# Performance work log

Hardware: AMD Instinct MI355X
Metric: run time of the kernel (lower is better)

The kernel has to match this reference:

```python
import jax, jax.numpy as jnp
import numpy as np


def _gat_layer(x, W, att_l, att_r, b, src, dst, num_nodes, heads, out_feat, concat):
    # x: [N, in], W: [in, H*F]
    xl = (x @ W).reshape(num_nodes, heads, out_feat)          # [N, H, F]
    a_l = jnp.sum(xl * att_l, axis=2)                          # [N, H]
    a_r = jnp.sum(xl * att_r, axis=2)                          # [N, H]
    # edge scores: alpha_j (source, att_l) + alpha_i (target, att_r)
    e = a_l[src] + a_r[dst]                                    # [E, H]
    e = jax.nn.leaky_relu(e, 0.2)
    # segment softmax over destination-node neighborhoods
    e_max = jax.ops.segment_max(e, dst, num_segments=num_nodes)
    e_exp = jnp.exp(e - e_max[dst])
    denom = jax.ops.segment_sum(e_exp, dst, num_segments=num_nodes)
    alpha = e_exp / (denom[dst] + 1e-16)                       # [E, H]
    # weighted gather + scatter-add aggregation
    msg = alpha[:, :, None] * xl[src]                          # [E, H, F]
    out = jax.ops.segment_sum(msg, dst, num_segments=num_nodes)  # [N, H, F]
    if concat:
        out = out.reshape(num_nodes, heads * out_feat)
    else:
        out = out.mean(axis=1)                                 # [N, F]
    return out + b


def setup_inputs() -> dict:
    key = jax.random.key(0)
    ks = jax.random.split(key, 8)
    N, E = 50000, 800000
    in_dim, hidden, out_dim, H = 128, 8, 64, 8
    x = jax.random.normal(ks[0], (N, in_dim), dtype=jnp.float32)
    edge_index = jax.random.randint(ks[1], (2, E), 0, N, dtype=jnp.int64)
    s = 0.1
    return {
        "x": x,
        "edge_index": edge_index,
        "W1": jax.random.normal(ks[2], (in_dim, hidden * H), dtype=jnp.float32) * s,
        "att_l1": jax.random.normal(ks[3], (1, H, hidden), dtype=jnp.float32) * s,
        "att_r1": jax.random.normal(ks[4], (1, H, hidden), dtype=jnp.float32) * s,
        "b1": jnp.zeros((hidden * H,), dtype=jnp.float32),
        "W2": jax.random.normal(ks[5], (hidden * H, out_dim * H), dtype=jnp.float32) * s,
        "att_l2": jax.random.normal(ks[6], (1, H, out_dim), dtype=jnp.float32) * s,
        "att_r2": jax.random.normal(ks[7], (1, H, out_dim), dtype=jnp.float32) * s,
        "b2": jnp.zeros((1, out_dim), dtype=jnp.float32),
    }


def reference(x, edge_index, W1, att_l1, att_r1, b1, W2, att_l2, att_r2, b2):
    N = x.shape[0]
    H = att_l1.shape[1]
    src, dst = edge_index[0], edge_index[1]
    h = _gat_layer(x, W1, att_l1, att_r1, b1, src, dst, N, H, att_l1.shape[2], concat=True)
    h = jax.nn.relu(h)
    out = _gat_layer(h, W2, att_l2, att_r2, b2, src, dst, N, H, att_l2.shape[2], concat=False)
    return out
```

## Files before the change

### kernel.cpp

```cpp
#include <hip/hip_runtime.h>
#include <stdint.h>

#define NT 256

typedef __attribute__((ext_vector_type(8))) short bf16x8;
typedef __attribute__((ext_vector_type(4))) float f32x4;

__device__ __forceinline__ float lrelu(float x) { return x > 0.f ? x : 0.2f * x; }

__device__ __forceinline__ float b2f(unsigned short u) {
  union { unsigned int i; float f; } v; v.i = ((unsigned int)u) << 16; return v.f;
}
__device__ __forceinline__ unsigned short f2b(float f) {
  unsigned int u = __float_as_uint(f);
  return (unsigned short)((u + 0x7fffu + ((u >> 16) & 1u)) >> 16);
}

__global__ void detect_kernel(const int* __restrict__ ei, int* __restrict__ flag, int twoE) {
  __shared__ int any;
  if (threadIdx.x == 0) any = 0;
  __syncthreads();
  int n = twoE < 4096 ? twoE : 4096;
  for (int i = threadIdx.x * 2 + 1; i < n; i += 2 * NT)
    if (ei[i] != 0) any = 1;
  __syncthreads();
  if (threadIdx.x == 0) *flag = any;
}

__global__ void cvt_edges_kernel(const void* __restrict__ ei, int* __restrict__ out,
                                 const int* __restrict__ flag, int* __restrict__ deg,
                                 int E, int twoE) {
  int i = blockIdx.x * NT + threadIdx.x;
  if (i >= twoE) return;
  int v;
  if (*flag) v = ((const int*)ei)[i];
  else       v = (int)((const long long*)ei)[i];
  out[i] = v;
  if (i >= E) atomicAdd(&deg[v], 1);
}

__global__ void zero2_kernel(int* __restrict__ a, int* __restrict__ b, int n) {
  int i = blockIdx.x * NT + threadIdx.x;
  if (i < n) { a[i] = 0; b[i] = 0; }
}

__global__ void scan1_kernel(const int* __restrict__ deg, int* __restrict__ bsum, int N) {
  __shared__ int sm[NT];
  int idx = blockIdx.x * NT + threadIdx.x;
  sm[threadIdx.x] = (idx < N) ? deg[idx] : 0;
  __syncthreads();
  for (int s = NT / 2; s > 0; s >>= 1) {
    if (threadIdx.x < s) sm[threadIdx.x] += sm[threadIdx.x + s];
    __syncthreads();
  }
  if (threadIdx.x == 0) bsum[blockIdx.x] = sm[0];
}

__global__ void scan2_kernel(const int* __restrict__ bsum, int* __restrict__ boff, int SB) {
  __shared__ int sm[NT];
  int t = threadIdx.x;
  int v = (t < SB) ? bsum[t] : 0;
  sm[t] = v;
  __syncthreads();
  for (int s = 1; s < NT; s <<= 1) {
    int add = (t >= s) ? sm[t - s] : 0;
    __syncthreads();
    sm[t] += add;
    __syncthreads();
  }
  if (t < SB) boff[t] = sm[t] - v;
}

__global__ void scan3_kernel(const int* __restrict__ deg, const int* __restrict__ boff,
                             int* __restrict__ rowptr, int N) {
  __shared__ int sm[NT];
  int idx = blockIdx.x * NT + threadIdx.x;
  int v = (idx < N) ? deg[idx] : 0;
  sm[threadIdx.x] = v;
  __syncthreads();
  for (int s = 1; s < NT; s <<= 1) {
    int add = (threadIdx.x >= s) ? sm[threadIdx.x - s] : 0;
    __syncthreads();
    sm[threadIdx.x] += add;
    __syncthreads();
  }
  if (idx <= N) rowptr[idx] = boff[blockIdx.x] + sm[threadIdx.x] - v;
}

__global__ void scatter_kernel(const int* __restrict__ src, const int* __restrict__ dst,
                               const int* __restrict__ rowptr, int* __restrict__ cursor,
                               int* __restrict__ csr_src, int E) {
  int e = blockIdx.x * NT + threadIdx.x;
  if (e >= E) return;
  int d = dst[e];
  int pos = rowptr[d] + atomicAdd(&cursor[d], 1);
  csr_src[pos] = src[e];
}

__global__ void foldB1_kernel(const float* __restrict__ W1, unsigned short* __restrict__ W1pack) {
  int idx = blockIdx.x * NT + threadIdx.x;
  if (idx >= 128 * 64) return;
  int j = idx & 7;
  int lane = (idx >> 3) & 63;
  int ctchunk = idx >> 9;
  int ct = ctchunk & 3;
  int chunk = ctchunk >> 2;
  int k = chunk * 32 + ((lane >> 4) << 3) + j;
  int col = ct * 16 + (lane & 15);
  W1pack[idx] = f2b(W1[k * 64 + col]);
}

__global__ void __launch_bounds__(NT)
gemm1_mfma_kernel(const float* __restrict__ x, const unsigned short* __restrict__ W1pack,
                  const float* __restrict__ attl, const float* __restrict__ attr,
                  unsigned short* __restrict__ xl1b, float* __restrict__ a1, int N) {
  int w = threadIdx.x >> 6;
  int lane = threadIdx.x & 63;
  int colb = lane & 15;
  int rgrp = lane >> 4;
  int row0w = blockIdx.x * 64 + w * 16;
  int arow = row0w + colb;
  if (arow >= N) arow = N - 1;
  const float* ap = x + (size_t)arow * 128 + (rgrp << 3);

  f32x4 acc[4];
#pragma unroll
  for (int ct = 0; ct < 4; ++ct) { acc[ct][0] = 0.f; acc[ct][1] = 0.f; acc[ct][2] = 0.f; acc[ct][3] = 0.f; }

#pragma unroll
  for (int chunk = 0; chunk < 4; ++chunk) {
    float4 v0 = *(const float4*)(ap + chunk * 32);
    float4 v1 = *(const float4*)(ap + chunk * 32 + 4);
    bf16x8 a;
    a[0] = (short)f2b(v0.x); a[1] = (short)f2b(v0.y);
    a[2] = (short)f2b(v0.z); a[3] = (short)f2b(v0.w);
    a[4] = (short)f2b(v1.x); a[5] = (short)f2b(v1.y);
    a[6] = (short)f2b(v1.z); a[7] = (short)f2b(v1.w);
    const unsigned short* bp = W1pack + ((size_t)chunk * 4 * 64 + lane) * 8;
#pragma unroll
    for (int ct = 0; ct < 4; ++ct) {
      bf16x8 b = *(const bf16x8*)(bp + (size_t)ct * 64 * 8);
      acc[ct] = __builtin_amdgcn_mfma_f32_16x16x32_bf16(a, b, acc[ct], 0, 0, 0);
    }
  }

#pragma unroll
  for (int ct = 0; ct < 4; ++ct) {
    float attlc = attl[ct * 16 + colb];
    float attrc = attr[ct * 16 + colb];
    int h = ct * 2 + (colb >> 3);
#pragma unroll
    for (int r = 0; r < 4; ++r) {
      int n = row0w + rgrp * 4 + r;
      float v = acc[ct][r];
      if (n < N) xl1b[(size_t)n * 64 + ct * 16 + colb] = f2b(v);
      float pl = v * attlc;
      float pr = v * attrc;
      pl += __shfl_xor(pl, 1, 64); pr += __shfl_xor(pr, 1, 64);
      pl += __shfl_xor(pl, 2, 64); pr += __shfl_xor(pr, 2, 64);
      pl += __shfl_xor(pl, 4, 64); pr += __shfl_xor(pr, 4, 64);
      if ((lane & 7) == 0 && n < N) {
        a1[n * 16 + h] = pl;
        a1[n * 16 + 8 + h] = pr;
      }
    }
  }
}

__global__ void foldw_kernel(const float* __restrict__ W2, const float* __restrict__ attl2,
                             const float* __restrict__ attr2, float* __restrict__ wl,
                             float* __restrict__ wr) {
  int t = threadIdx.x;
  int k = t >> 3, h = t & 7;
  float sl = 0.f, sr = 0.f;
  for (int f = 0; f < 64; ++f) {
    float w = W2[k * 512 + h * 64 + f];
    sl += w * attl2[h * 64 + f];
    sr += w * attr2[h * 64 + f];
  }
  wl[k * 8 + h] = sl;
  wr[k * 8 + h] = sr;
}

__global__ void foldB_kernel(const float* __restrict__ W2, unsigned short* __restrict__ Bpack) {
  int idx = blockIdx.x * NT + threadIdx.x;
  if (idx >= 512 * 64) return;
  int j = idx & 7;
  int lane = (idx >> 3) & 63;
  int ctchunk = idx >> 9;
  int ct = ctchunk & 3;
  int chunk = ctchunk >> 2;
  int hk = chunk * 32 + ((lane >> 4) << 3) + j;
  int h = hk >> 6, kk = hk & 63;
  int f = ct * 16 + (lane & 15);
  Bpack[idx] = f2b(W2[kk * 512 + h * 64 + f] * 0.125f);
}

__global__ void __launch_bounds__(NT)
node_aggr1_kernel(const int* __restrict__ rowptr, const int* __restrict__ csr_src,
                  const float* __restrict__ a1, const unsigned short* __restrict__ xl1b,
                  const float* __restrict__ b1, unsigned short* __restrict__ hrb, int N) {
  __shared__ float ps[4][64][8];
  __shared__ int ss[4][64];
  int w = threadIdx.x >> 6;
  int n = blockIdx.x * 4 + w;
  if (n >= N) return;
  int lane = threadIdx.x & 63;
  int hstage = lane & 7;
  int j8 = lane >> 3;
  int hown = lane >> 3;
  int base = rowptr[n];
  int deg = rowptr[n + 1] - base;

  float arh = a1[n * 16 + 8 + hstage];
  const unsigned short* xp = xl1b + lane;
  float acc = 0.f, dn = 0.f;

  for (int j0 = 0; j0 < deg; j0 += 64) {
    int cnt = deg - j0; if (cnt > 64) cnt = 64;
    if (lane < cnt) ss[w][lane] = csr_src[base + j0 + lane];
    asm volatile("s_waitcnt lgkmcnt(0)" ::: "memory");
    for (int jj = 0; jj < cnt; jj += 8) {
      int j = jj + j8;
      if (j < cnt) {
        int s = ss[w][j];
        float p = __expf(lrelu(a1[(unsigned)s * 16 + hstage] + arh));
        ps[w][j][hstage] = p;
      }
    }
    asm volatile("s_waitcnt lgkmcnt(0)" ::: "memory");
    int j = 0;
    for (; j + 4 <= cnt; j += 4) {
      int s0 = ss[w][j+0], s1 = ss[w][j+1], s2 = ss[w][j+2], s3 = ss[w][j+3];
      float p0 = ps[w][j+0][hown], p1 = ps[w][j+1][hown];
      float p2 = ps[w][j+2][hown], p3 = ps[w][j+3][hown];
      float v0 = b2f(xp[(unsigned)s0 * 64]), v1 = b2f(xp[(unsigned)s1 * 64]);
      float v2 = b2f(xp[(unsigned)s2 * 64]), v3 = b2f(xp[(unsigned)s3 * 64]);
      dn += (p0 + p1) + (p2 + p3);
      acc += p0 * v0 + p1 * v1 + p2 * v2 + p3 * v3;
    }
    for (; j < cnt; ++j) {
      int s = ss[w][j];
      float p = ps[w][j][hown];
      dn += p;
      acc += p * b2f(xp[(unsigned)s * 64]);
    }
  }
  acc = acc / (dn + 1e-16f);
  float hv = fmaxf(acc + b1[lane], 0.f);
  hrb[(size_t)n * 64 + lane] = f2b(hv);
}

#define A2N 256
__global__ void __launch_bounds__(NT)
a2dots_kernel(const unsigned short* __restrict__ hrb, const float* __restrict__ wl,
              const float* __restrict__ wr, float* __restrict__ a2, int N) {
  __shared__ unsigned short hs[A2N][65];
  __shared__ float wls[64 * 8], wrs[64 * 8];
  int tid = threadIdx.x;
  int n0 = blockIdx.x * A2N;
  for (int i = tid; i < 512; i += NT) { wls[i] = wl[i]; wrs[i] = wr[i]; }
  for (int i = tid; i < A2N * 8; i += NT) {
    int r = i >> 3, seg = i & 7;
    int n = n0 + r;
    uint4 v = make_uint4(0, 0, 0, 0);
    if (n < N) v = *(const uint4*)&hrb[(size_t)n * 64 + seg * 8];
    int c = seg * 8;
    hs[r][c + 0] = (unsigned short)(v.x);
    hs[r][c + 1] = (unsigned short)(v.x >> 16);
    hs[r][c + 2] = (unsigned short)(v.y);
    hs[r][c + 3] = (unsigned short)(v.y >> 16);
    hs[r][c + 4] = (unsigned short)(v.z);
    hs[r][c + 5] = (unsigned short)(v.z >> 16);
    hs[r][c + 6] = (unsigned short)(v.w);
    hs[r][c + 7] = (unsigned short)(v.w >> 16);
  }
  __syncthreads();
  float tl[8], tr[8];
#pragma unroll
  for (int h = 0; h < 8; ++h) { tl[h] = 0.f; tr[h] = 0.f; }
#pragma unroll 4
  for (int k = 0; k < 64; ++k) {
    float hv = b2f(hs[tid][k]);
    float4 l0 = *(const float4*)&wls[k * 8];
    float4 l1 = *(const float4*)&wls[k * 8 + 4];
    float4 r0 = *(const float4*)&wrs[k * 8];
    float4 r1 = *(const float4*)&wrs[k * 8 + 4];
    tl[0] += hv * l0.x; tl[1] += hv * l0.y; tl[2] += hv * l0.z; tl[3] += hv * l0.w;
    tl[4] += hv * l1.x; tl[5] += hv * l1.y; tl[6] += hv * l1.z; tl[7] += hv * l1.w;
    tr[0] += hv * r0.x; tr[1] += hv * r0.y; tr[2] += hv * r0.z; tr[3] += hv * r0.w;
    tr[4] += hv * r1.x; tr[5] += hv * r1.y; tr[6] += hv * r1.z; tr[7] += hv * r1.w;
  }
  int n = n0 + tid;
  if (n < N) {
    *(float4*)&a2[n * 16 + 0]  = make_float4(tl[0], tl[1], tl[2], tl[3]);
    *(float4*)&a2[n * 16 + 4]  = make_float4(tl[4], tl[5], tl[6], tl[7]);
    *(float4*)&a2[n * 16 + 8]  = make_float4(tr[0], tr[1], tr[2], tr[3]);
    *(float4*)&a2[n * 16 + 12] = make_float4(tr[4], tr[5], tr[6], tr[7]);
  }
}

__global__ void __launch_bounds__(NT)
node_aggr2_kernel(const int* __restrict__ rowptr, const int* __restrict__ csr_src,
                  const float* __restrict__ a2, const unsigned short* __restrict__ hrb,
                  unsigned short* __restrict__ gb, int N) {
  __shared__ float ps[4][64][8];
  __shared__ int ss[4][64];
  int w = threadIdx.x >> 6;
  int n = blockIdx.x * 4 + w;
  if (n >= N) return;
  int lane = threadIdx.x & 63;
  int hstage = lane & 7;
  int j8 = lane >> 3;
  int base = rowptr[n];
  int deg = rowptr[n + 1] - base;

  float arh = a2[n * 16 + 8 + hstage];
  const unsigned short* hp = hrb + lane;
  float acc[8] = {0.f, 0.f, 0.f, 0.f, 0.f, 0.f, 0.f, 0.f};
  float dn_own = 0.f;

  for (int j0 = 0; j0 < deg; j0 += 64) {
    int cnt = deg - j0; if (cnt > 64) cnt = 64;
    if (lane < cnt) ss[w][lane] = csr_src[base + j0 + lane];
    asm volatile("s_waitcnt lgkmcnt(0)" ::: "memory");
    for (int jj = 0; jj < cnt; jj += 8) {
      int j = jj + j8;
      if (j < cnt) {
        int s = ss[w][j];
        float p = __expf(lrelu(a2[(unsigned)s * 16 + hstage] + arh));
        ps[w][j][hstage] = p;
      }
    }
    asm volatile("s_waitcnt lgkmcnt(0)" ::: "memory");
    for (int j = 0; j < cnt; ++j) {
      int s = ss[w][j];
      float hv = b2f(hp[(unsigned)s * 64]);
      float4 pa = *(const float4*)&ps[w][j][0];
      float4 pb = *(const float4*)&ps[w][j][4];
      dn_own += ps[w][j][hstage];
      acc[0] += pa.x * hv; acc[1] += pa.y * hv; acc[2] += pa.z * hv; acc[3] += pa.w * hv;
      acc[4] += pb.x * hv; acc[5] += pb.y * hv; acc[6] += pb.z * hv; acc[7] += pb.w * hv;
    }
  }
#pragma unroll
  for (int h = 0; h < 8; ++h) {
    float dnh = __shfl(dn_own, h, 64);
    float v = acc[h] * (1.f / (dnh + 1e-16f));
    gb[(size_t)n * 512 + h * 64 + lane] = f2b(v);
  }
}

__global__ void __launch_bounds__(NT)
gemm3_mfma_kernel(const unsigned short* __restrict__ gb,
                  const unsigned short* __restrict__ Bpack,
                  const float* __restrict__ b2, float* __restrict__ out, int N) {
  int w = threadIdx.x >> 6;
  int lane = threadIdx.x & 63;
  int row0w = blockIdx.x * 64 + w * 16;
  int arow = row0w + (lane & 15);
  if (arow >= N) arow = N - 1;
  const unsigned short* ap = gb + (size_t)arow * 512 + ((lane >> 4) << 3);

  f32x4 acc[4];
#pragma unroll
  for (int ct = 0; ct < 4; ++ct) {
    float bb = b2[ct * 16 + (lane & 15)];
    acc[ct][0] = bb; acc[ct][1] = bb; acc[ct][2] = bb; acc[ct][3] = bb;
  }

#pragma unroll 4
  for (int chunk = 0; chunk < 16; ++chunk) {
    bf16x8 a = *(const bf16x8*)(ap + chunk * 32);
    const unsigned short* bp = Bpack + ((size_t)chunk * 4 * 64 + lane) * 8;
#pragma unroll
    for (int ct = 0; ct < 4; ++ct) {
      bf16x8 b = *(const bf16x8*)(bp + (size_t)ct * 64 * 8);
      acc[ct] = __builtin_amdgcn_mfma_f32_16x16x32_bf16(a, b, acc[ct], 0, 0, 0);
    }
  }

  int orow0 = row0w + ((lane >> 4) << 2);
#pragma unroll
  for (int ct = 0; ct < 4; ++ct) {
    int col = ct * 16 + (lane & 15);
#pragma unroll
    for (int r = 0; r < 4; ++r) {
      int n = orow0 + r;
      if (n < N) out[(size_t)n * 64 + col] = acc[ct][r];
    }
  }
}

extern "C" void kernel_launch(void* const* d_in, const int* in_sizes, int n_in,
                              void* d_out, int out_size, void* d_ws, size_t ws_size,
                              hipStream_t stream) {
  const float* x     = (const float*)d_in[0];
  const void*  ei    = d_in[1];
  const float* W1    = (const float*)d_in[2];
  const float* attl1 = (const float*)d_in[3];
  const float* attr1 = (const float*)d_in[4];
  const float* b1    = (const float*)d_in[5];
  const float* W2    = (const float*)d_in[6];
  const float* attl2 = (const float*)d_in[7];
  const float* attr2 = (const float*)d_in[8];
  const float* b2    = (const float*)d_in[9];
  float* out = (float*)d_out;

  int N = in_sizes[0] / 128;
  int E = in_sizes[1] / 2;

  char* ws = (char*)d_ws;
  size_t off = 0;
  auto alloc = [&](size_t bytes) {
    char* p = ws + off;
    off += (bytes + 255) & ~size_t(255);
    return p;
  };
  int*            edges   = (int*)alloc((size_t)2 * E * 4);
  int*            flag    = (int*)alloc(256);
  int*            deg     = (int*)alloc((size_t)N * 4);
  int*            cursor  = (int*)alloc((size_t)N * 4);
  int*            rowptr  = (int*)alloc((size_t)(N + 1) * 4);
  int*            bsum    = (int*)alloc(1024);
  int*            boff    = (int*)alloc(1024);
  int*            csr_src = (int*)alloc((size_t)E * 4);
  unsigned short* xl1b    = (unsigned short*)alloc((size_t)N * 64 * 2);
  float*          a1      = (float*)alloc((size_t)N * 16 * 4);
  unsigned short* hrb     = (unsigned short*)alloc((size_t)N * 64 * 2);
  float*          a2      = (float*)alloc((size_t)N * 16 * 4);
  float*          wl      = (float*)alloc(64 * 8 * 4);
  float*          wr      = (float*)alloc(64 * 8 * 4);
  unsigned short* Bpack   = (unsigned short*)alloc(512 * 64 * 2);
  unsigned short* W1pack  = (unsigned short*)alloc(128 * 64 * 2);
  unsigned short* gb      = (unsigned short*)alloc((size_t)N * 512 * 2);
  (void)ws_size;

  const int* srcp = edges;
  const int* dstp = edges + E;
  int SB = (N + 1 + NT - 1) / NT;

  detect_kernel<<<1, NT, 0, stream>>>((const int*)ei, flag, 2 * E);
  zero2_kernel<<<(N + NT - 1) / NT, NT, 0, stream>>>(deg, cursor, N);
  cvt_edges_kernel<<<(2 * E + NT - 1) / NT, NT, 0, stream>>>(ei, edges, flag, deg, E, 2 * E);

  scan1_kernel<<<SB, NT, 0, stream>>>(deg, bsum, N);
  scan2_kernel<<<1, NT, 0, stream>>>(bsum, boff, SB);
  scan3_kernel<<<SB, NT, 0, stream>>>(deg, boff, rowptr, N);
  scatter_kernel<<<(E + NT - 1) / NT, NT, 0, stream>>>(srcp, dstp, rowptr, cursor, csr_src, E);

  foldB1_kernel<<<(128 * 64 + NT - 1) / NT, NT, 0, stream>>>(W1, W1pack);
  gemm1_mfma_kernel<<<(N + 63) / 64, NT, 0, stream>>>(x, W1pack, attl1, attr1, xl1b, a1, N);
  foldw_kernel<<<1, 512, 0, stream>>>(W2, attl2, attr2, wl, wr);
  foldB_kernel<<<(512 * 64 + NT - 1) / NT, NT, 0, stream>>>(W2, Bpack);

  node_aggr1_kernel<<<(N + 3) / 4, NT, 0, stream>>>(rowptr, csr_src, a1, xl1b, b1, hrb, N);

  a2dots_kernel<<<(N + A2N - 1) / A2N, NT, 0, stream>>>(hrb, wl, wr, a2, N);

  node_aggr2_kernel<<<(N + 3) / 4, NT, 0, stream>>>(rowptr, csr_src, a2, hrb, gb, N);
  gemm3_mfma_kernel<<<(N + 63) / 64, NT, 0, stream>>>(gb, Bpack, b2, out, N);
}
```

Baseline: 233.7 us.

## Pre-bin edges by destination bucket before building CSR

Adds a two-pass coarse partition of the edges by destination block (dst>>8), using per-chunk histograms in shared memory, a scan and a binned write of packed (dst,src) pairs. The degree histogram and the CSR scatter then run over the binned array, so their atomics and writes touch nearby nodes instead of random ones. The degree count moves out of edge conversion into a separate kernel. This trades extra kernel launches and roughly three more passes over an 8-byte-per-edge buffer for better cache locality in the atomic scatter.

```diff
diff --git a/kernel.cpp b/kernel.cpp
--- a/kernel.cpp
+++ b/kernel.cpp
@@ -2,6 +2,8 @@
 #include <stdint.h>
 
 #define NT 256
+#define CHUNK 4096
+#define BSHIFT 8
 
 typedef __attribute__((ext_vector_type(8))) short bf16x8;
 typedef __attribute__((ext_vector_type(4))) float f32x4;
@@ -28,15 +30,11 @@
 }
 
 __global__ void cvt_edges_kernel(const void* __restrict__ ei, int* __restrict__ out,
-                                 const int* __restrict__ flag, int* __restrict__ deg,
-                                 int E, int twoE) {
+                                 const int* __restrict__ flag, int twoE) {
   int i = blockIdx.x * NT + threadIdx.x;
   if (i >= twoE) return;
-  int v;
-  if (*flag) v = ((const int*)ei)[i];
-  else       v = (int)((const long long*)ei)[i];
-  out[i] = v;
-  if (i >= E) atomicAdd(&deg[v], 1);
+  if (*flag) out[i] = ((const int*)ei)[i];
+  else       out[i] = (int)((const long long*)ei)[i];
 }
 
 __global__ void zero2_kernel(int* __restrict__ a, int* __restrict__ b, int n) {
@@ -44,10 +42,10 @@
   if (i < n) { a[i] = 0; b[i] = 0; }
 }
 
-__global__ void scan1_kernel(const int* __restrict__ deg, int* __restrict__ bsum, int N) {
+__global__ void scan1_kernel(const int* __restrict__ in, int* __restrict__ bsum, int n) {
   __shared__ int sm[NT];
   int idx = blockIdx.x * NT + threadIdx.x;
-  sm[threadIdx.x] = (idx < N) ? deg[idx] : 0;
+  sm[threadIdx.x] = (idx < n) ? in[idx] : 0;
   __syncthreads();
   for (int s = NT / 2; s > 0; s >>= 1) {
     if (threadIdx.x < s) sm[threadIdx.x] += sm[threadIdx.x + s];
@@ -71,11 +69,11 @@
   if (t < SB) boff[t] = sm[t] - v;
 }
 
-__global__ void scan3_kernel(const int* __restrict__ deg, const int* __restrict__ boff,
-                             int* __restrict__ rowptr, int N) {
+__global__ void scan3_kernel(const int* __restrict__ in, const int* __restrict__ boff,
+                             int* __restrict__ out, int n) {
   __shared__ int sm[NT];
   int idx = blockIdx.x * NT + threadIdx.x;
-  int v = (idx < N) ? deg[idx] : 0;
+  int v = (idx < n) ? in[idx] : 0;
   sm[threadIdx.x] = v;
   __syncthreads();
   for (int s = 1; s < NT; s <<= 1) {
@@ -84,17 +82,53 @@
     sm[threadIdx.x] += add;
     __syncthreads();
   }
-  if (idx <= N) rowptr[idx] = boff[blockIdx.x] + sm[threadIdx.x] - v;
-}
-
-__global__ void scatter_kernel(const int* __restrict__ src, const int* __restrict__ dst,
-                               const int* __restrict__ rowptr, int* __restrict__ cursor,
-                               int* __restrict__ csr_src, int E) {
+  if (idx <= n) out[idx] = boff[blockIdx.x] + sm[threadIdx.x] - v;
+}
+
+__global__ void bincount_kernel(const int* __restrict__ dst, int* __restrict__ blkcnt,
+                                int E, int nblk, int nbk) {
+  __shared__ int cnt[256];
+  int b = blockIdx.x;
+  for (int i = threadIdx.x; i < nbk; i += NT) cnt[i] = 0;
+  __syncthreads();
+  int beg = b * CHUNK;
+  int end = beg + CHUNK < E ? beg + CHUNK : E;
+  for (int i = beg + threadIdx.x; i < end; i += NT)
+    atomicAdd(&cnt[dst[i] >> BSHIFT], 1);
+  __syncthreads();
+  for (int i = threadIdx.x; i < nbk; i += NT) blkcnt[i * nblk + b] = cnt[i];
+}
+
+__global__ void binwrite_kernel(const int* __restrict__ src, const int* __restrict__ dst,
+                                const int* __restrict__ base, long long* __restrict__ binned,
+                                int E, int nblk, int nbk) {
+  __shared__ int cnt[256];
+  int b = blockIdx.x;
+  for (int i = threadIdx.x; i < nbk; i += NT) cnt[i] = base[i * nblk + b];
+  __syncthreads();
+  int beg = b * CHUNK;
+  int end = beg + CHUNK < E ? beg + CHUNK : E;
+  for (int i = beg + threadIdx.x; i < end; i += NT) {
+    int d = dst[i];
+    int pos = atomicAdd(&cnt[d >> BSHIFT], 1);
+    binned[pos] = ((long long)d << 32) | (unsigned int)src[i];
+  }
+}
+
+__global__ void deghist_kernel(const long long* __restrict__ binned, int* __restrict__ deg, int E) {
+  int e = blockIdx.x * NT + threadIdx.x;
+  if (e < E) atomicAdd(&deg[(int)(binned[e] >> 32)], 1);
+}
+
+__global__ void scatter2_kernel(const long long* __restrict__ binned, const int* __restrict__ rowptr,
+                                int* __restrict__ cursor, int* __restrict__ csr_src, int E) {
   int e = blockIdx.x * NT + threadIdx.x;
   if (e >= E) return;
-  int d = dst[e];
+  long long v = binned[e];
+  int d = (int)(v >> 32);
+  int s = (int)(v & 0xffffffffLL);
   int pos = rowptr[d] + atomicAdd(&cursor[d], 1);
-  csr_src[pos] = src[e];
+  csr_src[pos] = s;
 }
 
 __global__ void foldB1_kernel(const float* __restrict__ W1, unsigned short* __restrict__ W1pack) {
@@ -410,6 +444,10 @@
   int N = in_sizes[0] / 128;
   int E = in_sizes[1] / 2;
 
+  int nblk = (E + CHUNK - 1) / CHUNK;
+  int nbk  = (N + (1 << BSHIFT) - 1) >> BSHIFT;
+  int L    = nbk * nblk;
+
   char* ws = (char*)d_ws;
   size_t off = 0;
   auto alloc = [&](size_t bytes) {
@@ -424,6 +462,11 @@
   int*            rowptr  = (int*)alloc((size_t)(N + 1) * 4);
   int*            bsum    = (int*)alloc(1024);
   int*            boff    = (int*)alloc(1024);
+  int*            blkcnt  = (int*)alloc((size_t)L * 4);
+  int*            basebuf = (int*)alloc((size_t)(L + 1) * 4);
+  int*            bsum2   = (int*)alloc(1024);
+  int*            boff2   = (int*)alloc(1024);
+  long long*      binned  = (long long*)alloc((size_t)E * 8);
   int*            csr_src = (int*)alloc((size_t)E * 4);
   unsigned short* xl1b    = (unsigned short*)alloc((size_t)N * 64 * 2);
   float*          a1      = (float*)alloc((size_t)N * 16 * 4);
@@ -438,16 +481,25 @@
 
   const int* srcp = edges;
   const int* dstp = edges + E;
-  int SB = (N + 1 + NT - 1) / NT;
+  int SB  = (N + 1 + NT - 1) / NT;
+  int SBL = (L + 1 + NT - 1) / NT;
 
   detect_kernel<<<1, NT, 0, stream>>>((const int*)ei, flag, 2 * E);
+  cvt_edges_kernel<<<(2 * E + NT - 1) / NT, NT, 0, stream>>>(ei, edges, flag, 2 * E);
   zero2_kernel<<<(N + NT - 1) / NT, NT, 0, stream>>>(deg, cursor, N);
-  cvt_edges_kernel<<<(2 * E + NT - 1) / NT, NT, 0, stream>>>(ei, edges, flag, deg, E, 2 * E);
-
+
+  bincount_kernel<<<nblk, NT, 0, stream>>>(dstp, blkcnt, E, nblk, nbk);
+  scan1_kernel<<<SBL, NT, 0, stream>>>(blkcnt, bsum2, L);
+  scan2_kernel<<<1, NT, 0, stream>>>(bsum2, boff2, SBL);
+  scan3_kernel<<<SBL, NT, 0, stream>>>(blkcnt, boff2, basebuf, L);
+  binwrite_kernel<<<nblk, NT, 0, stream>>>(srcp, dstp, basebuf, binned, E, nblk, nbk);
+
+  deghist_kernel<<<(E + NT - 1) / NT, NT, 0, stream>>>(binned, deg, E);
   scan1_kernel<<<SB, NT, 0, stream>>>(deg, bsum, N);
   scan2_kernel<<<1, NT, 0, stream>>>(bsum, boff, SB);
   scan3_kernel<<<SB, NT, 0, stream>>>(deg, boff, rowptr, N);
-  scatter_kernel<<<(E + NT - 1) / NT, NT, 0, stream>>>(srcp, dstp, rowptr, cursor, csr_src, E);
+
+  scatter2_kernel<<<(E + NT - 1) / NT, NT, 0, stream>>>(binned, rowptr, cursor, csr_src, E);
 
   foldB1_kernel<<<(128 * 64 + NT - 1) / NT, NT, 0, stream>>>(W1, W1pack);
   gemm1_mfma_kernel<<<(N + 63) / 64, NT, 0, stream>>>(x, W1pack, attl1, attr1, xl1b, a1, N);
```

After: 219.6 us. 1.06x faster.
